# Kernel optimization log

Hardware: AMD Instinct MI355X
Metric: run time of the kernel (lower is better)

The kernel has to match this reference:

```python
import jax, jax.numpy as jnp
import numpy as np
import math

V, D, H, FF, L, S, B = 32000, 1024, 16, 4096, 8, 1024, 4
HD = D // H


def _pos_encoding(seq_len, dim):
    pos = np.arange(seq_len)[:, None].astype(np.float32)
    div = np.exp(np.arange(0, dim, 2).astype(np.float32) * -(math.log(10000.0) / dim))
    pe = np.zeros((seq_len, dim), dtype=np.float32)
    pe[:, 0::2] = np.sin(pos * div)
    pe[:, 1::2] = np.cos(pos * div)
    return jnp.asarray(pe)


def setup_inputs() -> dict:
    key = jax.random.key(0)
    ks = jax.random.split(key, 24)
    sc = 0.02
    inp = {
        'tokens': jax.random.randint(ks[0], (B, S), 0, V),
        'emb_W': jax.random.normal(ks[1], (V, D), jnp.float32) * sc,
        'Wq': jax.random.normal(ks[2], (L, D, D), jnp.float32) * sc,
        'bq': jnp.zeros((L, D), jnp.float32),
        'Wk': jax.random.normal(ks[3], (L, D, D), jnp.float32) * sc,
        'bk': jnp.zeros((L, D), jnp.float32),
        'Wv': jax.random.normal(ks[4], (L, D, D), jnp.float32) * sc,
        'bv': jnp.zeros((L, D), jnp.float32),
        'Wo': jax.random.normal(ks[5], (L, D, D), jnp.float32) * sc,
        'bo': jnp.zeros((L, D), jnp.float32),
        'ln1_g': jnp.ones((L, D), jnp.float32),
        'ln1_b': jnp.zeros((L, D), jnp.float32),
        'ln2_g': jnp.ones((L, D), jnp.float32),
        'ln2_b': jnp.zeros((L, D), jnp.float32),
        'W1': jax.random.normal(ks[6], (L, D, FF), jnp.float32) * sc,
        'b1': jnp.zeros((L, FF), jnp.float32),
        'W2': jax.random.normal(ks[7], (L, FF, D), jnp.float32) * sc,
        'b2': jnp.zeros((L, D), jnp.float32),
        'lnf_g': jnp.ones((D,), jnp.float32),
        'lnf_b': jnp.zeros((D,), jnp.float32),
        'head_W': jax.random.normal(ks[8], (D, V), jnp.float32) * sc,
        'head_b': jnp.zeros((V,), jnp.float32),
    }
    return inp


def _layernorm(x, g, b, eps=1e-5):
    mu = jnp.mean(x, axis=-1, keepdims=True)
    var = jnp.mean(jnp.square(x - mu), axis=-1, keepdims=True)
    return (x - mu) * jax.lax.rsqrt(var + eps) * g + b


def _attention(x, Wq, bq, Wk, bk, Wv, bv, Wo, bo, causal_mask):
    b, s, d = x.shape
    q = (x @ Wq + bq).reshape(b, s, H, HD).transpose(0, 2, 1, 3)
    k = (x @ Wk + bk).reshape(b, s, H, HD).transpose(0, 2, 1, 3)
    v = (x @ Wv + bv).reshape(b, s, H, HD).transpose(0, 2, 1, 3)
    scores = jnp.einsum('bhqd,bhkd->bhqk', q, k) / math.sqrt(HD)
    scores = jnp.where(causal_mask, scores, -1e9)
    attn = jax.nn.softmax(scores, axis=-1)
    out = jnp.einsum('bhqk,bhkd->bhqd', attn, v)
    out = out.transpose(0, 2, 1, 3).reshape(b, s, d)
    return out @ Wo + bo


def reference(tokens, emb_W, Wq, bq, Wk, bk, Wv, bv, Wo, bo,
              ln1_g, ln1_b, ln2_g, ln2_b, W1, b1, W2, b2,
              lnf_g, lnf_b, head_W, head_b):
    b, s = tokens.shape
    mask = jnp.tril(jnp.ones((s, s), bool))[None, None]  # (1,1,s,s)
    x = emb_W[tokens] + _pos_encoding(s, D)[None]
    for l in range(L):
        a = _attention(_layernorm(x, ln1_g[l], ln1_b[l]),
                       Wq[l], bq[l], Wk[l], bk[l], Wv[l], bv[l], Wo[l], bo[l], mask)
        x = x + a
        h = _layernorm(x, ln2_g[l], ln2_b[l])
        h = jax.nn.relu(h @ W1[l] + b1[l]) @ W2[l] + b2[l]
        x = x + h
    x = _layernorm(x, lnf_g, lnf_b)
    return x @ head_W + head_b
```

## Files before the change

kernel.cpp:

```cpp
#include <hip/hip_runtime.h>
#include <math.h>


using u16 = unsigned short;
using u32 = unsigned int;
typedef __attribute__((ext_vector_type(4))) float  f32x4;
typedef __attribute__((ext_vector_type(8))) short  s16x8;
typedef __attribute__((ext_vector_type(8))) __bf16 bf16x8;

__device__ __forceinline__ u16 f2bf(float f) {
  u32 u = __builtin_bit_cast(u32, f);
  u += 0x7fffu + ((u >> 16) & 1u);
  return (u16)(u >> 16);
}

__device__ __forceinline__ f32x4 mfma16(s16x8 a, s16x8 b, f32x4 c) {
  return __builtin_amdgcn_mfma_f32_16x16x32_bf16(
      __builtin_bit_cast(bf16x8, a), __builtin_bit_cast(bf16x8, b), c, 0, 0, 0);
}

#define GLD16(gp, lp) __builtin_amdgcn_global_load_lds(                    \
    (const __attribute__((address_space(1))) void*)(gp),                   \
    (__attribute__((address_space(3))) void*)(lp), 16, 0, 0)

__global__ __launch_bounds__(256) void transpose_cvt(
    const float* __restrict__ in, u16* __restrict__ out,
    int C, long long inLS, long long outLS, int outRS)
{
  __shared__ float t[32][33];
  int tr = threadIdx.x >> 5, tc = threadIdx.x & 31;
  const float* ip = in + (size_t)blockIdx.z * inLS +
                    ((size_t)blockIdx.x * 32 + tr) * C + blockIdx.y * 32 + tc;
#pragma unroll
  for (int p = 0; p < 4; ++p) t[p * 8 + tr][tc] = ip[(size_t)p * 8 * C];
  __syncthreads();
  u16* op = out + (size_t)blockIdx.z * outLS +
            ((size_t)blockIdx.y * 32 + tr) * outRS + (size_t)blockIdx.x * 32 + tc;
#pragma unroll
  for (int p = 0; p < 4; ++p) op[(size_t)p * 8 * outRS] = f2bf(t[tc][p * 8 + tr]);
}

__global__ __launch_bounds__(256) void pack_bqkv(
    const float* __restrict__ bq, const float* __restrict__ bk,
    const float* __restrict__ bv, float* __restrict__ outb)
{
  int i = blockIdx.x * 256 + threadIdx.x;
  int ly = i / 3072, j = i % 3072;
  float v = (j < 1024) ? bq[ly * 1024 + j]
          : (j < 2048) ? bk[ly * 1024 + (j - 1024)]
                       : bv[ly * 1024 + (j - 2048)];
  outb[i] = v;
}

__global__ __launch_bounds__(256) void embed_kernel(
    const int* __restrict__ tokens, const float* __restrict__ embW,
    float* __restrict__ x)
{
  int row = blockIdx.x;
  int s = row & 1023;
  int tok = tokens[row];
  int d0 = threadIdx.x * 4;
  float4 e = *(const float4*)&embW[(size_t)tok * 1024 + d0];
  const float c = -9.210340371976184f / 1024.0f;
  float div0 = expf((float)d0 * c);
  float div1 = expf((float)(d0 + 2) * c);
  float sn0, cs0, sn1, cs1;
  sincosf((float)s * div0, &sn0, &cs0);
  sincosf((float)s * div1, &sn1, &cs1);
  float4 r;
  r.x = e.x + sn0; r.y = e.y + cs0; r.z = e.z + sn1; r.w = e.w + cs1;
  *(float4*)&x[(size_t)row * 1024 + d0] = r;
}

__global__ __launch_bounds__(256) void ln_kernel(
    const float* __restrict__ x, const float* __restrict__ g,
    const float* __restrict__ b, u16* __restrict__ y)
{
  int row = blockIdx.x, tid = threadIdx.x;
  float4 v = *(const float4*)&x[(size_t)row * 1024 + tid * 4];
  float sum = v.x + v.y + v.z + v.w;
  float sq = v.x * v.x + v.y * v.y + v.z * v.z + v.w * v.w;
#pragma unroll
  for (int o = 32; o > 0; o >>= 1) {
    sum += __shfl_xor(sum, o, 64);
    sq  += __shfl_xor(sq,  o, 64);
  }
  __shared__ float ps[8];
  int w = tid >> 6;
  if ((tid & 63) == 0) { ps[w] = sum; ps[4 + w] = sq; }
  __syncthreads();
  sum = ps[0] + ps[1] + ps[2] + ps[3];
  sq  = ps[4] + ps[5] + ps[6] + ps[7];
  float mu = sum * (1.0f / 1024.0f);
  float var = sq * (1.0f / 1024.0f) - mu * mu;
  float rs = rsqrtf(var + 1e-5f);
  float4 gg = *(const float4*)&g[tid * 4];
  float4 bb = *(const float4*)&b[tid * 4];
  u32 lo = (u32)f2bf((v.x - mu) * rs * gg.x + bb.x) |
           ((u32)f2bf((v.y - mu) * rs * gg.y + bb.y) << 16);
  u32 hi = (u32)f2bf((v.z - mu) * rs * gg.z + bb.z) |
           ((u32)f2bf((v.w - mu) * rs * gg.w + bb.w) << 16);
  uint2 o2; o2.x = lo; o2.y = hi;
  *(uint2*)&y[(size_t)row * 1024 + tid * 4] = o2;
}

template<int OMODE, int RELU, int BYMAJ>
__global__ __launch_bounds__(512, 2) void gemm256(
    const u16* __restrict__ A, const u16* __restrict__ Bt,
    const float* __restrict__ bias, void* Cp, int M, int N, int K, int gd)
{
  __shared__ alignas(16) u16 lds[2][32768];
  const int tid = threadIdx.x;
  const int w = tid >> 6, l = tid & 63;
  const int g = l >> 4, lr = l & 15;
  const int wm = w >> 2, wn = w & 3;
  int nwg = gridDim.x;
  int bid = blockIdx.x;
  int swz = (bid & 7) * (nwg >> 3) + (bid >> 3);
  int bx, by;
  if (BYMAJ) { by = swz % gd; bx = swz / gd; }
  else       { bx = swz % gd; by = swz / gd; }
  int m0 = by << 8, n0 = bx << 8;

  const u16* Ag[4]; const u16* Bg[4]; int dstE[4];
#pragma unroll
  for (int s2 = 0; s2 < 4; ++s2) {
    int idx = s2 * 512 + tid;
    int row = idx >> 3;
    int ch = (idx & 7) ^ (row & 7);
    Ag[s2] = A  + (size_t)(m0 + row) * K + ch * 8;
    Bg[s2] = Bt + (size_t)(n0 + row) * K + ch * 8;
    dstE[s2] = idx * 8;
  }
  const int colx0 = ((g)     ^ (lr & 7)) * 8;
  const int colx1 = ((4 + g) ^ (lr & 7)) * 8;
  const int abase = (wm * 128 + lr) * 64;
  const int bbase = 16384 + (wn * 64 + lr) * 64;

  f32x4 acc[8][4];
#pragma unroll
  for (int i = 0; i < 8; ++i)
#pragma unroll
    for (int j = 0; j < 4; ++j) acc[i][j] = f32x4{0.f, 0.f, 0.f, 0.f};

  const int nk = K >> 6;
#pragma unroll
  for (int s2 = 0; s2 < 4; ++s2) GLD16(Ag[s2], &lds[0][dstE[s2]]);
#pragma unroll
  for (int s2 = 0; s2 < 4; ++s2) GLD16(Bg[s2], &lds[0][16384 + dstE[s2]]);
  asm volatile("s_waitcnt vmcnt(0)" ::: "memory");
  __builtin_amdgcn_s_barrier();

  int cur = 0;
  for (int t = 0; t < nk; ++t) {
    const bool more = (t + 1 < nk);
    if (more) {
      const int kn = (t + 1) << 6;
#pragma unroll
      for (int s2 = 0; s2 < 4; ++s2) GLD16(Ag[s2] + kn, &lds[cur ^ 1][dstE[s2]]);
#pragma unroll
      for (int s2 = 0; s2 < 4; ++s2) GLD16(Bg[s2] + kn, &lds[cur ^ 1][16384 + dstE[s2]]);
    }
    s16x8 a0[8], b0[4], a1[8], b1[4];
#pragma unroll
    for (int mf = 0; mf < 8; ++mf) a0[mf] = *(const s16x8*)&lds[cur][abase + mf * 1024 + colx0];
#pragma unroll
    for (int nf = 0; nf < 4; ++nf) b0[nf] = *(const s16x8*)&lds[cur][bbase + nf * 1024 + colx0];
#pragma unroll
    for (int mf = 0; mf < 8; ++mf) a1[mf] = *(const s16x8*)&lds[cur][abase + mf * 1024 + colx1];
#pragma unroll
    for (int nf = 0; nf < 4; ++nf) b1[nf] = *(const s16x8*)&lds[cur][bbase + nf * 1024 + colx1];
    __builtin_amdgcn_s_setprio(1);
#pragma unroll
    for (int mf = 0; mf < 8; ++mf)
#pragma unroll
      for (int nf = 0; nf < 4; ++nf) acc[mf][nf] = mfma16(a0[mf], b0[nf], acc[mf][nf]);
#pragma unroll
    for (int mf = 0; mf < 8; ++mf)
#pragma unroll
      for (int nf = 0; nf < 4; ++nf) acc[mf][nf] = mfma16(a1[mf], b1[nf], acc[mf][nf]);
    __builtin_amdgcn_s_setprio(0);
    if (more) {
      asm volatile("s_waitcnt vmcnt(0)" ::: "memory");
      __builtin_amdgcn_s_barrier();
      cur ^= 1;
    }
  }

  float* fst = (float*)(void*)&lds[0][0];
#pragma unroll
  for (int mf = 0; mf < 8; ++mf) {
    __builtin_amdgcn_s_barrier();
#pragma unroll
    for (int nf = 0; nf < 4; ++nf) {
      int cl = wn * 64 + nf * 16 + lr;
      float bv = bias[n0 + cl];
      int rl = wm * 16 + g * 4;
#pragma unroll
      for (int r = 0; r < 4; ++r) {
        float v = acc[mf][nf][r] + bv;
        if (RELU) v = fmaxf(v, 0.f);
        fst[(rl + r) * 260 + cl] = v;
      }
    }
    __builtin_amdgcn_s_barrier();
    if (OMODE == 0) {
#pragma unroll
      for (int it = 0; it < 2; ++it) {
        int seg = it * 512 + tid;
        int row = seg >> 5;
        int co  = (seg & 31) * 8;
        int grow = m0 + (row >> 4) * 128 + mf * 16 + (row & 15);
        const float* src = &fst[row * 260 + co];
        uint4 q;
        q.x = (u32)f2bf(src[0]) | ((u32)f2bf(src[1]) << 16);
        q.y = (u32)f2bf(src[2]) | ((u32)f2bf(src[3]) << 16);
        q.z = (u32)f2bf(src[4]) | ((u32)f2bf(src[5]) << 16);
        q.w = (u32)f2bf(src[6]) | ((u32)f2bf(src[7]) << 16);
        *(uint4*)&((u16*)Cp)[(size_t)grow * N + n0 + co] = q;
      }
    } else {
#pragma unroll
      for (int it = 0; it < 4; ++it) {
        int seg = it * 512 + tid;
        int row = seg >> 6;
        int co  = (seg & 63) * 4;
        int grow = m0 + (row >> 4) * 128 + mf * 16 + (row & 15);
        f32x4 q = *(const f32x4*)&fst[row * 260 + co];
        *(f32x4*)&((float*)Cp)[(size_t)grow * N + n0 + co] = q;
      }
    }
  }
}

template<int OMODE, int RELU>
__global__ __launch_bounds__(256, 3) void gemm_p(
    const u16* __restrict__ A, const u16* __restrict__ Bt,
    const float* __restrict__ bias, const float* res, void* Cp,
    int M, int N, int K, int gx)
{
  __shared__ alignas(16) u16 lds[2][8192];
  const int tid = threadIdx.x;
  const int w = tid >> 6, l = tid & 63;
  const int g = l >> 4, lr = l & 15;
  const int wm = w >> 1, wn = w & 1;
  int nwg = gridDim.x;
  int bid = blockIdx.x;
  int swz = (bid & 7) * (nwg >> 3) + (bid >> 3);
  int bx = swz % gx, by = swz / gx;
  int m0 = by << 7, n0 = bx << 7;

  const u16 *Ag[2], *Bg[2];
  int dstA[2], dstB[2];
#pragma unroll
  for (int s = 0; s < 2; ++s) {
    int idx = s * 256 + tid;
    int row = idx >> 2;
    int ch = (idx & 3) ^ ((row >> 1) & 3);
    Ag[s] = A  + (size_t)(m0 + row) * K + ch * 8;
    Bg[s] = Bt + (size_t)(n0 + row) * K + ch * 8;
    dstA[s] = idx * 8;
    dstB[s] = 4096 + idx * 8;
  }
  const int colx = (g ^ ((lr >> 1) & 3)) * 8;
  const int aoff = (wm * 64 + lr) * 32 + colx;
  const int boff = 4096 + (wn * 64 + lr) * 32 + colx;

  f32x4 acc[4][4];
#pragma unroll
  for (int i = 0; i < 4; ++i)
#pragma unroll
    for (int j = 0; j < 4; ++j) acc[i][j] = f32x4{0.f, 0.f, 0.f, 0.f};

  const int nk = K >> 5;
#pragma unroll
  for (int s = 0; s < 2; ++s) GLD16(Ag[s], &lds[0][dstA[s]]);
#pragma unroll
  for (int s = 0; s < 2; ++s) GLD16(Bg[s], &lds[0][dstB[s]]);
  asm volatile("s_waitcnt vmcnt(0)" ::: "memory");
  __builtin_amdgcn_s_barrier();

  int cur = 0;
  s16x8 aC[4], bC[4];
#pragma unroll
  for (int i = 0; i < 4; ++i) aC[i] = *(const s16x8*)&lds[0][aoff + i * 512];
#pragma unroll
  for (int j = 0; j < 4; ++j) bC[j] = *(const s16x8*)&lds[0][boff + j * 512];

  for (int t = 0; t < nk; ++t) {
    const bool more = (t + 1 < nk);
    if (more) {
      const int kn = (t + 1) << 5;
#pragma unroll
      for (int s = 0; s < 2; ++s) GLD16(Ag[s] + kn, &lds[cur ^ 1][dstA[s]]);
#pragma unroll
      for (int s = 0; s < 2; ++s) GLD16(Bg[s] + kn, &lds[cur ^ 1][dstB[s]]);
    }
    __builtin_amdgcn_s_setprio(1);
#pragma unroll
    for (int i = 0; i < 4; ++i)
#pragma unroll
      for (int j = 0; j < 4; ++j) acc[i][j] = mfma16(aC[i], bC[j], acc[i][j]);
    __builtin_amdgcn_s_setprio(0);
    if (more) {
      asm volatile("s_waitcnt vmcnt(0)" ::: "memory");
      __builtin_amdgcn_s_barrier();
      cur ^= 1;
#pragma unroll
      for (int i = 0; i < 4; ++i) aC[i] = *(const s16x8*)&lds[cur][aoff + i * 512];
#pragma unroll
      for (int j = 0; j < 4; ++j) bC[j] = *(const s16x8*)&lds[cur][boff + j * 512];
    }
  }
#pragma unroll
  for (int mf = 0; mf < 4; ++mf) {
    int row = m0 + wm * 64 + mf * 16 + g * 4;
#pragma unroll
    for (int nf = 0; nf < 4; ++nf) {
      int col = n0 + wn * 64 + nf * 16 + lr;
      float bv = bias[col];
#pragma unroll
      for (int r = 0; r < 4; ++r) {
        float v = acc[mf][nf][r] + bv;
        if (RELU) v = fmaxf(v, 0.f);
        size_t idx = (size_t)(row + r) * N + col;
        if (OMODE == 0)      ((u16*)Cp)[idx] = f2bf(v);
        else if (OMODE == 1) ((float*)Cp)[idx] = v + res[idx];
        else                 ((float*)Cp)[idx] = v;
      }
    }
  }
}

__global__ __launch_bounds__(256) void attn_kernel(
    const u16* __restrict__ qkv, u16* __restrict__ outp)
{
  int b = blockIdx.x >> 4, h = blockIdx.x & 15;
  int q0 = blockIdx.y << 6;
  int tid = threadIdx.x, w = tid >> 6, l = tid & 63;
  int g = l >> 4, lr = l & 15;
  const int RS = 3072;
  const u16* base = qkv + (size_t)b * 1024 * RS + h * 64;
  const u16* Qb = base;
  const u16* Kb = base + 1024;
  const u16* Vb = base + 2048;
  __shared__ alignas(16) u16 Plds[4][1024];
  __shared__ alignas(16) u16 Vt[4096];
  char* Pw = (char*)&Plds[w][0];

  s16x8 qf[2];
#pragma unroll
  for (int ks = 0; ks < 2; ++ks)
    qf[ks] = *(const s16x8*)&Qb[(size_t)(q0 + w * 16 + lr) * RS + ks * 32 + g * 8];

  f32x4 o[4];
#pragma unroll
  for (int n = 0; n < 4; ++n) o[n] = f32x4{0.f, 0.f, 0.f, 0.f};
  float mr[4] = {-INFINITY, -INFINITY, -INFINITY, -INFINITY};
  float ls[4] = {0.f, 0.f, 0.f, 0.f};

  int ntile = (q0 >> 6) + 1;
  for (int kt = 0; kt < ntile; ++kt) {
    int kv0 = kt << 6;
    f32x4 sc[4];
#pragma unroll
    for (int t = 0; t < 4; ++t) sc[t] = f32x4{0.f, 0.f, 0.f, 0.f};
#pragma unroll
    for (int ks = 0; ks < 2; ++ks)
#pragma unroll
      for (int t = 0; t < 4; ++t) {
        s16x8 kf = *(const s16x8*)&Kb[(size_t)(kv0 + t * 16 + lr) * RS + ks * 32 + g * 8];
        sc[t] = mfma16(qf[ks], kf, sc[t]);
      }
#pragma unroll
    for (int p = 0; p < 2; ++p) {
      int key = p * 32 + (tid >> 3);
      int d0 = (tid & 7) * 8;
      s16x8 vrow = *(const s16x8*)&Vb[(size_t)(kv0 + key) * RS + d0];
#pragma unroll
      for (int j = 0; j < 8; ++j) {
        int d = d0 + j;
        int byt = (d * 128 + key * 2) ^ ((d & 7) << 4);
        *(u16*)((char*)Vt + byt) = (u16)vrow[j];
      }
    }
    float p4[4][4];
    float tmax[4] = {-INFINITY, -INFINITY, -INFINITY, -INFINITY};
    int qr_base = q0 + w * 16 + g * 4;
#pragma unroll
    for (int t = 0; t < 4; ++t) {
      int key = kv0 + t * 16 + lr;
#pragma unroll
      for (int r = 0; r < 4; ++r) {
        float s = sc[t][r] * 0.125f;
        s = (key <= qr_base + r) ? s : -1e30f;
        p4[t][r] = s;
        tmax[r] = fmaxf(tmax[r], s);
      }
    }
#pragma unroll
    for (int off = 1; off < 16; off <<= 1)
#pragma unroll
      for (int r = 0; r < 4; ++r) tmax[r] = fmaxf(tmax[r], __shfl_xor(tmax[r], off, 64));
    float corr[4], rsum[4];
#pragma unroll
    for (int r = 0; r < 4; ++r) {
      float mn = fmaxf(mr[r], tmax[r]);
      corr[r] = __expf(mr[r] - mn);
      mr[r] = mn;
      rsum[r] = 0.f;
    }
#pragma unroll
    for (int t = 0; t < 4; ++t)
#pragma unroll
      for (int r = 0; r < 4; ++r) {
        float e = __expf(p4[t][r] - mr[r]);
        p4[t][r] = e;
        rsum[r] += e;
      }
#pragma unroll
    for (int off = 1; off < 16; off <<= 1)
#pragma unroll
      for (int r = 0; r < 4; ++r) rsum[r] += __shfl_xor(rsum[r], off, 64);
#pragma unroll
    for (int r = 0; r < 4; ++r) ls[r] = ls[r] * corr[r] + rsum[r];
#pragma unroll
    for (int n = 0; n < 4; ++n)
#pragma unroll
      for (int r = 0; r < 4; ++r) o[n][r] *= corr[r];
#pragma unroll
    for (int t = 0; t < 4; ++t)
#pragma unroll
      for (int r = 0; r < 4; ++r) {
        int prow = g * 4 + r;
        int byt = (prow * 128 + (t * 16 + lr) * 2) ^ ((prow & 7) << 4);
        *(u16*)(Pw + byt) = f2bf(p4[t][r]);
      }
    __syncthreads();
#pragma unroll
    for (int ks = 0; ks < 2; ++ks) {
      int ab = (lr * 128 + ks * 64 + g * 16) ^ ((lr & 7) << 4);
      s16x8 pa = *(const s16x8*)(Pw + ab);
#pragma unroll
      for (int n = 0; n < 4; ++n) {
        int vb2 = ((n * 16 + lr) * 128 + ks * 64 + g * 16) ^ ((lr & 7) << 4);
        s16x8 vfr = *(const s16x8*)((const char*)Vt + vb2);
        o[n] = mfma16(pa, vfr, o[n]);
      }
    }
    __syncthreads();
  }
#pragma unroll
  for (int n = 0; n < 4; ++n)
#pragma unroll
    for (int r = 0; r < 4; ++r) {
      float v = o[n][r] / ls[r];
      outp[(size_t)(b * 1024 + q0 + w * 16 + g * 4 + r) * 1024 + h * 64 + n * 16 + lr] = f2bf(v);
    }
}

extern "C" void kernel_launch(void* const* d_in, const int* in_sizes, int n_in,
                              void* d_out, int out_size, void* d_ws, size_t ws_size,
                              hipStream_t stream)
{
  const int*   tokens = (const int*)  d_in[0];
  const float* embW   = (const float*)d_in[1];
  const float* Wq     = (const float*)d_in[2];
  const float* bq     = (const float*)d_in[3];
  const float* Wk     = (const float*)d_in[4];
  const float* bk     = (const float*)d_in[5];
  const float* Wv     = (const float*)d_in[6];
  const float* bv     = (const float*)d_in[7];
  const float* Wo     = (const float*)d_in[8];
  const float* bo     = (const float*)d_in[9];
  const float* ln1g   = (const float*)d_in[10];
  const float* ln1b   = (const float*)d_in[11];
  const float* ln2g   = (const float*)d_in[12];
  const float* ln2b   = (const float*)d_in[13];
  const float* W1     = (const float*)d_in[14];
  const float* b1     = (const float*)d_in[15];
  const float* W2     = (const float*)d_in[16];
  const float* b2     = (const float*)d_in[17];
  const float* lnfg   = (const float*)d_in[18];
  const float* lnfb   = (const float*)d_in[19];
  const float* headW  = (const float*)d_in[20];
  const float* headb  = (const float*)d_in[21];
  (void)in_sizes; (void)n_in; (void)out_size;

  char* ws = (char*)d_ws;
  u16*   qkvT = (u16*)(ws);
  u16*   woT  = (u16*)(ws + 50331648);
  u16*   w1T  = (u16*)(ws + 67108864);
  u16*   w2T  = (u16*)(ws + 134217728);
  u16*   headT= (u16*)(ws + 201326592);
  float* bqkv = (float*)(ws + 266862592);
  float* x    = (float*)(ws + 266960896);
  u16*   y    = (u16*)(ws + 283738112);
  u16*   qkv  = (u16*)(ws + 292126720);
  u16*   attno= (u16*)(ws + 317292544);
  u16*   h1   = (u16*)(ws + 325681152);
  if (ws_size < 359235584ull) return;

  dim3 blk(256);
  dim3 blk5(512);
  transpose_cvt<<<dim3(32, 32, 8),  blk, 0, stream>>>(Wq, qkvT,           1024,  1048576LL, 3145728LL, 1024);
  transpose_cvt<<<dim3(32, 32, 8),  blk, 0, stream>>>(Wk, qkvT + 1048576, 1024,  1048576LL, 3145728LL, 1024);
  transpose_cvt<<<dim3(32, 32, 8),  blk, 0, stream>>>(Wv, qkvT + 2097152, 1024,  1048576LL, 3145728LL, 1024);
  transpose_cvt<<<dim3(32, 32, 8),  blk, 0, stream>>>(Wo, woT,            1024,  1048576LL, 1048576LL, 1024);
  transpose_cvt<<<dim3(32, 128, 8), blk, 0, stream>>>(W1, w1T,            4096,  4194304LL, 4194304LL, 1024);
  transpose_cvt<<<dim3(128, 32, 8), blk, 0, stream>>>(W2, w2T,            1024,  4194304LL, 4194304LL, 4096);
  transpose_cvt<<<dim3(32, 1000, 1),blk, 0, stream>>>(headW, headT,       32000, 0LL,       0LL,       1024);
  pack_bqkv<<<96, blk, 0, stream>>>(bq, bk, bv, bqkv);
  embed_kernel<<<4096, blk, 0, stream>>>(tokens, embW, x);
  for (int ly = 0; ly < 8; ++ly) {
    ln_kernel<<<4096, blk, 0, stream>>>(x, ln1g + ly * 1024, ln1b + ly * 1024, y);
    gemm256<0, 0, 0><<<192, blk5, 0, stream>>>(y, qkvT + (size_t)ly * 3145728,
        bqkv + ly * 3072, qkv, 4096, 3072, 1024, 12);
    attn_kernel<<<dim3(64, 16), blk, 0, stream>>>(qkv, attno);
    gemm_p<1, 0><<<256, blk, 0, stream>>>(attno, woT + (size_t)ly * 1048576,
        bo + ly * 1024, x, x, 4096, 1024, 1024, 8);
    ln_kernel<<<4096, blk, 0, stream>>>(x, ln2g + ly * 1024, ln2b + ly * 1024, y);
    gemm256<0, 1, 0><<<256, blk5, 0, stream>>>(y, w1T + (size_t)ly * 4194304,
        b1 + ly * 4096, h1, 4096, 4096, 1024, 16);
    gemm_p<1, 0><<<256, blk, 0, stream>>>(h1, w2T + (size_t)ly * 4194304,
        b2 + ly * 1024, x, x, 4096, 1024, 4096, 8);
  }
  ln_kernel<<<4096, blk, 0, stream>>>(x, lnfg, lnfb, y);
  gemm256<2, 0, 1><<<2000, blk5, 0, stream>>>(y, headT, headb,
      (float*)d_out, 4096, 32000, 1024, 16);
}
```

Baseline: 2.681 ms.

## Split-K the FF2 GEMM with a reduce kernel and remap GEMM tiles per XCD

The FF2 projection (K=4096) now runs on the 256x256 gemm256 kernel split four ways along K. Each split writes fp32 partials to a new workspace buffer, and an ff2_reduce kernel adds the partials, the bias and the residual. The block-to-tile mapping for the QKV, FF1 and head GEMMs is rewritten so that each XCD gets a 4x8 group of tiles, which should improve L2 reuse. The QKV and head launches are padded to multiples of the group size, and out-of-range blocks exit early. Split-K adds about 64MB of partial-sum traffic plus an extra launch, and it only runs if the workspace is large enough; otherwise the old path is used.

```diff
diff --git a/kernel.cpp b/kernel.cpp
--- a/kernel.cpp
+++ b/kernel.cpp
@@ -104,23 +104,50 @@
   *(uint2*)&y[(size_t)row * 1024 + tid * 4] = o2;
 }
 
-template<int OMODE, int RELU, int BYMAJ>
+__global__ __launch_bounds__(256) void ff2_reduce(
+    const float* __restrict__ p, const float* __restrict__ b2,
+    float* __restrict__ x)
+{
+  int row = blockIdx.x, c = threadIdx.x * 4;
+  size_t idx = (size_t)row * 1024 + c;
+  f32x4 v  = *(f32x4*)&x[idx];
+  f32x4 a0 = *(const f32x4*)&p[idx];
+  f32x4 a1 = *(const f32x4*)&p[idx + 4194304];
+  f32x4 a2 = *(const f32x4*)&p[idx + 8388608];
+  f32x4 a3 = *(const f32x4*)&p[idx + 12582912];
+  f32x4 bb = *(const f32x4*)&b2[c];
+  v = v + a0 + a1 + a2 + a3 + bb;
+  *(f32x4*)&x[idx] = v;
+}
+
+template<int OMODE, int RELU, int MAP>
 __global__ __launch_bounds__(512, 2) void gemm256(
-    const u16* __restrict__ A, const u16* __restrict__ Bt,
-    const float* __restrict__ bias, void* Cp, int M, int N, int K, int gd)
+    const u16* __restrict__ A, int lda, const u16* __restrict__ Bt,
+    const float* __restrict__ bias, void* Cp, int M, int N, int klen,
+    int gxp8, int gxreal)
 {
   __shared__ alignas(16) u16 lds[2][32768];
   const int tid = threadIdx.x;
   const int w = tid >> 6, l = tid & 63;
   const int g = l >> 4, lr = l & 15;
   const int wm = w >> 2, wn = w & 3;
-  int nwg = gridDim.x;
-  int bid = blockIdx.x;
-  int swz = (bid & 7) * (nwg >> 3) + (bid >> 3);
-  int bx, by;
-  if (BYMAJ) { by = swz % gd; bx = swz / gd; }
-  else       { bx = swz % gd; by = swz / gd; }
-  int m0 = by << 8, n0 = bx << 8;
+  const int bid = blockIdx.x;
+  const int xcd = bid & 7, k = bid >> 3;
+  int by, bx, split = 0;
+  if (MAP == 0) {
+    int t = k >> 5, j = k & 31;
+    int s = xcd + 8 * t;
+    by = (s / gxp8) * 4 + (j & 3);
+    bx = (s % gxp8) * 8 + (j >> 2);
+    if (bx >= gxreal) return;
+  } else {
+    split = bid & 3;
+    by = (bid >> 2) & 15;
+    bx = bid >> 6;
+  }
+  const int m0 = by << 8, n0 = bx << 8;
+  const u16* Ab = A  + (split << 10);
+  const u16* Bb = Bt + (split << 10);
 
   const u16* Ag[4]; const u16* Bg[4]; int dstE[4];
 #pragma unroll
@@ -128,8 +155,8 @@
     int idx = s2 * 512 + tid;
     int row = idx >> 3;
     int ch = (idx & 7) ^ (row & 7);
-    Ag[s2] = A  + (size_t)(m0 + row) * K + ch * 8;
-    Bg[s2] = Bt + (size_t)(n0 + row) * K + ch * 8;
+    Ag[s2] = Ab + (size_t)(m0 + row) * lda + ch * 8;
+    Bg[s2] = Bb + (size_t)(n0 + row) * lda + ch * 8;
     dstE[s2] = idx * 8;
   }
   const int colx0 = ((g)     ^ (lr & 7)) * 8;
@@ -141,9 +168,9 @@
 #pragma unroll
   for (int i = 0; i < 8; ++i)
 #pragma unroll
-    for (int j = 0; j < 4; ++j) acc[i][j] = f32x4{0.f, 0.f, 0.f, 0.f};
-
-  const int nk = K >> 6;
+    for (int j2 = 0; j2 < 4; ++j2) acc[i][j2] = f32x4{0.f, 0.f, 0.f, 0.f};
+
+  const int nk = klen >> 6;
 #pragma unroll
   for (int s2 = 0; s2 < 4; ++s2) GLD16(Ag[s2], &lds[0][dstE[s2]]);
 #pragma unroll
@@ -188,13 +215,17 @@
   }
 
   float* fst = (float*)(void*)&lds[0][0];
+  float* Cf = (OMODE == 3)
+            ? ((float*)Cp + (size_t)split * ((size_t)M * N))
+            : (float*)Cp;
 #pragma unroll
   for (int mf = 0; mf < 8; ++mf) {
     __builtin_amdgcn_s_barrier();
 #pragma unroll
     for (int nf = 0; nf < 4; ++nf) {
       int cl = wn * 64 + nf * 16 + lr;
-      float bv = bias[n0 + cl];
+      float bv = 0.f;
+      if (OMODE != 3) bv = bias[n0 + cl];
       int rl = wm * 16 + g * 4;
 #pragma unroll
       for (int r = 0; r < 4; ++r) {
@@ -227,7 +258,7 @@
         int co  = (seg & 63) * 4;
         int grow = m0 + (row >> 4) * 128 + mf * 16 + (row & 15);
         f32x4 q = *(const f32x4*)&fst[row * 260 + co];
-        *(f32x4*)&((float*)Cp)[(size_t)grow * N + n0 + co] = q;
+        *(f32x4*)&Cf[(size_t)grow * N + n0 + co] = q;
       }
     }
   }
@@ -499,7 +530,9 @@
   u16*   qkv  = (u16*)(ws + 292126720);
   u16*   attno= (u16*)(ws + 317292544);
   u16*   h1   = (u16*)(ws + 325681152);
+  float* pbuf = (float*)(ws + 359235584);
   if (ws_size < 359235584ull) return;
+  const bool splitk = (ws_size >= 426344448ull);
 
   dim3 blk(256);
   dim3 blk5(512);
@@ -514,18 +547,27 @@
   embed_kernel<<<4096, blk, 0, stream>>>(tokens, embW, x);
   for (int ly = 0; ly < 8; ++ly) {
     ln_kernel<<<4096, blk, 0, stream>>>(x, ln1g + ly * 1024, ln1b + ly * 1024, y);
-    gemm256<0, 0, 0><<<192, blk5, 0, stream>>>(y, qkvT + (size_t)ly * 3145728,
-        bqkv + ly * 3072, qkv, 4096, 3072, 1024, 12);
+    gemm256<0, 0, 0><<<256, blk5, 0, stream>>>(y, 1024,
+        qkvT + (size_t)ly * 3145728, bqkv + ly * 3072, qkv,
+        4096, 3072, 1024, 2, 12);
     attn_kernel<<<dim3(64, 16), blk, 0, stream>>>(qkv, attno);
     gemm_p<1, 0><<<256, blk, 0, stream>>>(attno, woT + (size_t)ly * 1048576,
         bo + ly * 1024, x, x, 4096, 1024, 1024, 8);
     ln_kernel<<<4096, blk, 0, stream>>>(x, ln2g + ly * 1024, ln2b + ly * 1024, y);
-    gemm256<0, 1, 0><<<256, blk5, 0, stream>>>(y, w1T + (size_t)ly * 4194304,
-        b1 + ly * 4096, h1, 4096, 4096, 1024, 16);
-    gemm_p<1, 0><<<256, blk, 0, stream>>>(h1, w2T + (size_t)ly * 4194304,
-        b2 + ly * 1024, x, x, 4096, 1024, 4096, 8);
+    gemm256<0, 1, 0><<<256, blk5, 0, stream>>>(y, 1024,
+        w1T + (size_t)ly * 4194304, b1 + ly * 4096, h1,
+        4096, 4096, 1024, 2, 16);
+    if (splitk) {
+      gemm256<3, 0, 1><<<256, blk5, 0, stream>>>(h1, 4096,
+          w2T + (size_t)ly * 4194304, nullptr, pbuf,
+          4096, 1024, 1024, 0, 0);
+      ff2_reduce<<<4096, blk, 0, stream>>>(pbuf, b2 + ly * 1024, x);
+    } else {
+      gemm_p<1, 0><<<256, blk, 0, stream>>>(h1, w2T + (size_t)ly * 4194304,
+          b2 + ly * 1024, x, x, 4096, 1024, 4096, 8);
+    }
   }
   ln_kernel<<<4096, blk, 0, stream>>>(x, lnfg, lnfb, y);
-  gemm256<2, 0, 1><<<2000, blk5, 0, stream>>>(y, headT, headb,
-      (float*)d_out, 4096, 32000, 1024, 16);
-}
+  gemm256<2, 0, 0><<<2048, blk5, 0, stream>>>(y, 1024, headT, headb,
+      (float*)d_out, 4096, 32000, 1024, 16, 125);
+}
```

New measurement: 2.349 ms. 1.14x faster.
